# Kernel tuning notes

Measured on AMD Instinct MI355X. Metric: run time of the kernel, lower is better.

## Reference

```python
import jax, jax.numpy as jnp
import numpy as np

G = 8          # n_games
D_IN = 512     # per-game input dim (equal for all games)
H1 = 1024
H2 = 1024
A = 128        # max_actions
B = 8192       # batch rows


def setup_inputs() -> dict:
    key = jax.random.key(0)
    ks = jax.random.split(key, 9)
    state = jax.random.normal(ks[0], (B, D_IN), dtype=jnp.float32)
    idx = jax.random.randint(ks[1], (B,), 0, G, dtype=jnp.int32)
    # per-game input linears: uniform(-1/sqrt(fan_in), 1/sqrt(fan_in))
    lim1 = 1.0 / np.sqrt(D_IN)
    W1 = jax.random.uniform(ks[2], (G, D_IN, H1), minval=-lim1, maxval=lim1, dtype=jnp.float32)
    b1 = jax.random.uniform(ks[3], (G, H1), minval=-lim1, maxval=lim1, dtype=jnp.float32)
    # shared linear
    lim2 = 1.0 / np.sqrt(H1)
    W2 = jax.random.uniform(ks[4], (H1, H2), minval=-lim2, maxval=lim2, dtype=jnp.float32)
    b2 = jax.random.uniform(ks[5], (H2,), minval=-lim2, maxval=lim2, dtype=jnp.float32)
    # per-game output heads: uniform(-0.003, 0.003)
    W3 = jax.random.uniform(ks[6], (G, H2, A), minval=-0.003, maxval=0.003, dtype=jnp.float32)
    b3 = jax.random.uniform(ks[7], (G, A), minval=-0.003, maxval=0.003, dtype=jnp.float32)
    return {"state": state, "idx": idx, "W1": W1, "b1": b1, "W2": W2, "b2": b2, "W3": W3, "b3": b3}


def reference(state, idx, W1, b1, W2, b2, W3, b3):
    # Torch code concatenates per-game groups in sorted-unique-idx order,
    # i.e. a stable permutation of rows by idx; reproduce exactly.
    perm = jnp.argsort(idx, stable=True)          # [B]
    s = state[perm]                               # [B, D_IN]
    g = idx[perm]                                 # [B] game of each permuted row
    # routed first layer: compute all games then gather per-row game
    h1_all = jnp.einsum('bd,gdh->bgh', s, W1) + b1            # [B, G, H1]
    h1 = jax.nn.relu(jnp.take_along_axis(h1_all, g[:, None, None], axis=1)[:, 0, :])  # [B, H1]
    h_f = jax.nn.relu(h1 @ W2 + b2)                            # [B, H2]
    a = jnp.tanh(jnp.einsum('bh,gha->bga', h_f, W3) + b3)      # [B, G, A]
    # NOTE: original gathers heads with the ORIGINAL (unpermuted) idx,
    # even though rows of `a` are in permuted order. Reproduce faithfully.
    out = jnp.take_along_axis(a, idx[:, None, None], axis=1)[:, 0, :]  # [B, A]
    return out
```

## Files before the change

### kernel.cpp

```cpp
#include <hip/hip_runtime.h>
#include <math.h>

#define G_GAMES 8
#define D_IN 512
#define H1 1024
#define H2 1024
#define A_DIM 128
#define B_ROWS 8192

typedef short bf16x8 __attribute__((ext_vector_type(8)));
typedef float f32x4 __attribute__((ext_vector_type(4)));

#define WS_OFF   0u
#define WS_PERM  256u
#define WS_SPERM 33280u
#define WS_W1T   (WS_SPERM + B_ROWS*D_IN*2u)
#define WS_W2T   (WS_W1T + G_GAMES*D_IN*H1*2u)
#define WS_W3T   (WS_W2T + (unsigned)H1*H2*2u)
#define WS_H1    (WS_W3T + G_GAMES*H2*A_DIM*2u)
#define WS_HF    WS_SPERM

__device__ __forceinline__ unsigned short f2bf(float x) {
  union { float f; unsigned int u; } v; v.f = x;
  unsigned int r = v.u + 0x7fffu + ((v.u >> 16) & 1u);
  return (unsigned short)(r >> 16);
}

__device__ __forceinline__ unsigned int cvt_pk_bf16(float lo, float hi) {
  unsigned int r;
  asm("v_cvt_pk_bf16_f32 %0, %1, %2" : "=v"(r) : "v"(lo), "v"(hi));
  return r;
}

__device__ __forceinline__ void async_load16(const void* gptr, void* ldsptr) {
  __builtin_amdgcn_global_load_lds(
      (const __attribute__((address_space(1))) unsigned int*)gptr,
      (__attribute__((address_space(3))) unsigned int*)ldsptr,
      16, 0, 0);
}

__device__ void sort_256(const int* __restrict__ idx, int* __restrict__ perm,
                         int* __restrict__ off) {
  __shared__ int wtot[4][9];
  __shared__ int wbase[4][9];
  __shared__ int offs[9];
  const int t = threadIdx.x, lane = t & 63, wave = t >> 6;
  int my[32];
#pragma unroll
  for (int i = 0; i < 8; ++i) {
    const int4 a = *(const int4*)(idx + t * 32 + i * 4);
    my[i*4+0] = a.x; my[i*4+1] = a.y; my[i*4+2] = a.z; my[i*4+3] = a.w;
  }
  int local[8];
#pragma unroll
  for (int g = 0; g < 8; ++g) {
    int c = 0;
#pragma unroll
    for (int i = 0; i < 32; ++i) c += (my[i] == g) ? 1 : 0;
    local[g] = c;
  }
  int incl[8];
#pragma unroll
  for (int g = 0; g < 8; ++g) {
    int v = local[g];
#pragma unroll
    for (int d = 1; d < 64; d <<= 1) {
      const int n = __shfl_up(v, d);
      if (lane >= d) v += n;
    }
    incl[g] = v;
  }
  if (lane == 63) {
#pragma unroll
    for (int g = 0; g < 8; ++g) wtot[wave][g] = incl[g];
  }
  __syncthreads();
  if (t < 8) {
    int s = 0;
#pragma unroll
    for (int w = 0; w < 4; ++w) { wbase[w][t] = s; s += wtot[w][t]; }
    wtot[0][t] = s;
  }
  __syncthreads();
  if (t == 0) {
    int s = 0;
#pragma unroll
    for (int g = 0; g < 8; ++g) { offs[g] = s; off[g] = s; s += wtot[0][g]; }
    offs[8] = s; off[8] = s;
  }
  __syncthreads();
#pragma unroll
  for (int g = 0; g < 8; ++g) {
    int sg = offs[g] + wbase[wave][g] + (incl[g] - local[g]);
#pragma unroll
    for (int i = 0; i < 32; ++i) {
      const bool m = (my[i] == g);
      if (m) perm[sg] = t * 32 + i;
      sg += m ? 1 : 0;
    }
  }
}

__device__ void trans_tile(const float* __restrict__ in,
                           unsigned short* __restrict__ out,
                           int R, int C, int xt, int yt, int z) {
  in  += (size_t)z * R * C;
  out += (size_t)z * R * C;
  __shared__ unsigned short tl[64][68];
  const int c0 = xt * 64, r0 = yt * 64;
  const int t = threadIdx.x;
#pragma unroll
  for (int pass = 0; pass < 4; ++pass) {
    const int id = pass * 256 + t;
    const int r = id >> 4, f4c = (id & 15) << 2;
    const float4 v = *(const float4*)(in + (size_t)(r0 + r) * C + c0 + f4c);
    uint2 w;
    w.x = cvt_pk_bf16(v.x, v.y);
    w.y = cvt_pk_bf16(v.z, v.w);
    *(uint2*)&tl[r][f4c] = w;
  }
  __syncthreads();
#pragma unroll
  for (int pass = 0; pass < 2; ++pass) {
    const int cc = t >> 2, k0 = ((t & 3) << 3) + (pass << 5);
    unsigned short u[8];
#pragma unroll
    for (int j = 0; j < 8; ++j) u[j] = tl[k0 + j][cc];
    uint4 v;
    v.x = (unsigned)u[0] | ((unsigned)u[1] << 16);
    v.y = (unsigned)u[2] | ((unsigned)u[3] << 16);
    v.z = (unsigned)u[4] | ((unsigned)u[5] << 16);
    v.w = (unsigned)u[6] | ((unsigned)u[7] << 16);
    *(uint4*)(out + (size_t)(c0 + cc) * R + r0 + k0) = v;
  }
}

__global__ __launch_bounds__(256) void k_pre1(const float* __restrict__ W1,
                                              const float* __restrict__ W2,
                                              const float* __restrict__ W3,
                                              const int* __restrict__ idx,
                                              unsigned short* __restrict__ W1T,
                                              unsigned short* __restrict__ W2T,
                                              unsigned short* __restrict__ W3T,
                                              int* __restrict__ perm,
                                              int* __restrict__ off) {
  const int b = blockIdx.x;
  if (b < 1024) {
    const int z = b >> 7, r = b & 127;
    trans_tile(W1, W1T, D_IN, H1, r & 15, r >> 4, z);
  } else if (b < 1280) {
    const int r = b - 1024;
    trans_tile(W2, W2T, H1, H2, r & 15, r >> 4, 0);
  } else if (b < 1536) {
    const int r = (b - 1280) & 31, z = (b - 1280) >> 5;
    trans_tile(W3, W3T, H2, A_DIM, r & 1, r >> 1, z);
  } else {
    sort_256(idx, perm, off);
  }
}

template <int KTOT>
__device__ __forceinline__ void gemm_db_core(const unsigned short* const* aP,
                                             const unsigned short* const* bP,
                                             char* smem, int tid, f32x4 acc[4][4]) {
  const int lane = tid & 63, wave = tid >> 6;
  const int wm = wave & 1, wn = wave >> 1;
  const int sw = lane & 15, quad = lane >> 4;
  const int mA = wm * 64 + sw;
  const int nB = wn * 64 + sw;
  char* A0 = smem;          char* A1 = smem + 16384;
  char* B0 = smem + 32768;  char* B1 = smem + 49152;
  const int NIT = KTOT >> 6;
#pragma unroll
  for (int c = 0; c < 4; ++c) {
    async_load16(aP[c], A0 + (wave * 32 + c * 8) * 128);
    async_load16(bP[c], B0 + (wave * 32 + c * 8) * 128);
  }
#pragma unroll 2
  for (int k = 0; k < NIT; ++k) {
    __syncthreads();
    char* A = (k & 1) ? A1 : A0;
    char* B = (k & 1) ? B1 : B0;
    if (k + 1 < NIT) {
      char* An = (k & 1) ? A0 : A1;
      char* Bn = (k & 1) ? B0 : B1;
      const int koff = (k + 1) << 6;
#pragma unroll
      for (int c = 0; c < 4; ++c) {
        async_load16(aP[c] + koff, An + (wave * 32 + c * 8) * 128);
        async_load16(bP[c] + koff, Bn + (wave * 32 + c * 8) * 128);
      }
    }
#pragma unroll
    for (int ks = 0; ks < 2; ++ks) {
      const int u = ((((ks << 2) + quad) ^ (sw & 7)) << 4);
      bf16x8 aF[4], bF[4];
#pragma unroll
      for (int i = 0; i < 4; ++i) {
        aF[i] = *(const bf16x8*)(A + (mA + i * 16) * 128 + u);
        bF[i] = *(const bf16x8*)(B + (nB + i * 16) * 128 + u);
      }
#pragma unroll
      for (int i = 0; i < 4; ++i)
#pragma unroll
        for (int j = 0; j < 4; ++j)
          acc[i][j] = __builtin_amdgcn_mfma_f32_16x16x32_bf16(aF[i], bF[j], acc[i][j], 0, 0, 0);
    }
  }
}

__device__ __forceinline__ bool seg_map(const int* __restrict__ off, int T,
                                        int& g, int& seg1, int& row0) {
  int base = 0;
  for (int gg = 0; gg < 8; ++gg) {
    const int s = off[gg], e = off[gg + 1];
    const int nt = (e - s + 127) >> 7;
    if (T < base + nt) { g = gg; seg1 = e; row0 = s + (T - base) * 128; return true; }
    base += nt;
  }
  return false;
}

__device__ __forceinline__ bool seg_map32(const int* __restrict__ off, int T,
                                          int& g, int& seg1, int& row0) {
  int base = 0;
  for (int gg = 0; gg < 8; ++gg) {
    const int s = off[gg], e = off[gg + 1];
    const int nt = (e - s + 31) >> 5;
    if (T < base + nt) { g = gg; seg1 = e; row0 = s + (T - base) * 32; return true; }
    base += nt;
  }
  return false;
}

__device__ __forceinline__ void epilogue_bf16(char* smem, const f32x4 acc[4][4],
                                              const float* bj, int tid,
                                              unsigned short* __restrict__ outp,
                                              size_t ldOut, int row0, int col0,
                                              int vrows) {
  const int lane = tid & 63, wave = tid >> 6;
  const int wm = wave & 1, wn = wave >> 1;
  const int sw = lane & 15, quad = lane >> 4;
  __syncthreads();
#pragma unroll
  for (int i = 0; i < 4; ++i)
#pragma unroll
    for (int j = 0; j < 4; ++j)
#pragma unroll
      for (int r = 0; r < 4; ++r) {
        const int row = wm * 64 + i * 16 + quad * 4 + r;
        const int col = wn * 64 + j * 16 + sw;
        const float v = fmaxf(acc[i][j][r] + bj[j], 0.0f);
        *(unsigned short*)(smem + row * 264 + col * 2) = f2bf(v);
      }
  __syncthreads();
#pragma unroll
  for (int q = 0; q < 8; ++q) {
    const int idxq = q * 256 + tid;
    const int row = idxq >> 4, ch = idxq & 15;
    if (row < vrows) {
      const uint2 lo = *(const uint2*)(smem + row * 264 + ch * 16);
      const uint2 hi = *(const uint2*)(smem + row * 264 + ch * 16 + 8);
      uint4 v; v.x = lo.x; v.y = lo.y; v.z = hi.x; v.w = hi.y;
      *(uint4*)((char*)outp + ((size_t)(row0 + row) * ldOut + col0 + ch * 8) * 2) = v;
    }
  }
}

__global__ __launch_bounds__(256, 2) void k_gemm1(const float* __restrict__ state,
                                                  const int* __restrict__ perm,
                                                  const unsigned short* __restrict__ W1T,
                                                  const float* __restrict__ b1,
                                                  const int* __restrict__ off,
                                                  unsigned short* __restrict__ h1out) {
  __shared__ __align__(16) char smem[65536];
  int g, seg1, row0;
  if (!seg_map(off, blockIdx.x, g, seg1, row0)) return;
  const int col0 = blockIdx.y * 128;
  const int tid = threadIdx.x, lane = tid & 63, wave = tid >> 6;
  const int wm = wave & 1, wn = wave >> 1;
  const int sw = lane & 15, quad = lane >> 4;
  const int lc = lane & 7;
  const int gcol = ((lane & 7) ^ (lane >> 3)) << 3;
  const float* aS[4];
  int ldsA[4];
  const unsigned short* bP[4];
#pragma unroll
  for (int c = 0; c < 4; ++c) {
    const int rl = wave * 32 + c * 8 + (lane >> 3);
    int p = row0 + rl;
    if (p > seg1 - 1) p = seg1 - 1;
    aS[c]  = state + (size_t)perm[p] * D_IN + lc * 8;
    ldsA[c] = rl * 128 + ((lc ^ (rl & 7)) << 4);
    bP[c]  = W1T + (size_t)g * H1 * D_IN + (size_t)(col0 + rl) * D_IN + gcol;
  }
  char* A0 = smem;          char* A1 = smem + 16384;
  char* B0 = smem + 32768;  char* B1 = smem + 49152;
  const int mA = wm * 64 + sw, nB = wn * 64 + sw;
  f32x4 acc[4][4] = {};
  {
    float4 t0[4], t1[4];
#pragma unroll
    for (int c = 0; c < 4; ++c) {
      t0[c] = *(const float4*)(aS[c]);
      t1[c] = *(const float4*)(aS[c] + 4);
      async_load16(bP[c], B0 + (wave * 32 + c * 8) * 128);
    }
#pragma unroll
    for (int c = 0; c < 4; ++c) {
      uint4 pk;
      pk.x = cvt_pk_bf16(t0[c].x, t0[c].y);
      pk.y = cvt_pk_bf16(t0[c].z, t0[c].w);
      pk.z = cvt_pk_bf16(t1[c].x, t1[c].y);
      pk.w = cvt_pk_bf16(t1[c].z, t1[c].w);
      *(uint4*)(A0 + ldsA[c]) = pk;
    }
  }
  const int NIT = D_IN >> 6;
#pragma unroll 2
  for (int k = 0; k < NIT; ++k) {
    __syncthreads();
    char* A = (k & 1) ? A1 : A0;
    char* B = (k & 1) ? B1 : B0;
    float4 t0[4], t1[4];
    const bool pf = (k + 1 < NIT);
    if (pf) {
      char* Bn = (k & 1) ? B0 : B1;
      const int koff = (k + 1) << 6;
#pragma unroll
      for (int c = 0; c < 4; ++c) {
        t0[c] = *(const float4*)(aS[c] + koff);
        t1[c] = *(const float4*)(aS[c] + koff + 4);
        async_load16(bP[c] + koff, Bn + (wave * 32 + c * 8) * 128);
      }
    }
#pragma unroll
    for (int ks = 0; ks < 2; ++ks) {
      const int u = ((((ks << 2) + quad) ^ (sw & 7)) << 4);
      bf16x8 aF[4], bF[4];
#pragma unroll
      for (int i = 0; i < 4; ++i) {
        aF[i] = *(const bf16x8*)(A + (mA + i * 16) * 128 + u);
        bF[i] = *(const bf16x8*)(B + (nB + i * 16) * 128 + u);
      }
#pragma unroll
      for (int i = 0; i < 4; ++i)
#pragma unroll
        for (int j = 0; j < 4; ++j)
          acc[i][j] = __builtin_amdgcn_mfma_f32_16x16x32_bf16(aF[i], bF[j], acc[i][j], 0, 0, 0);
    }
    if (pf) {
      char* An = (k & 1) ? A0 : A1;
#pragma unroll
      for (int c = 0; c < 4; ++c) {
        uint4 pk;
        pk.x = cvt_pk_bf16(t0[c].x, t0[c].y);
        pk.y = cvt_pk_bf16(t0[c].z, t0[c].w);
        pk.z = cvt_pk_bf16(t1[c].x, t1[c].y);
        pk.w = cvt_pk_bf16(t1[c].z, t1[c].w);
        *(uint4*)(An + ldsA[c]) = pk;
      }
    }
  }
  const float* bg = b1 + g * H1;
  float bj[4];
#pragma unroll
  for (int j = 0; j < 4; ++j) bj[j] = bg[col0 + wn * 64 + j * 16 + sw];
  const int vrows = min(128, seg1 - row0);
  epilogue_bf16(smem, acc, bj, tid, h1out, H1, row0, col0, vrows);
}

__global__ __launch_bounds__(256) void k_gemm2(const unsigned short* __restrict__ h1in,
                                               const unsigned short* __restrict__ W2T,
                                               const float* __restrict__ b2,
                                               unsigned short* __restrict__ hfout) {
  __shared__ __align__(16) char smem[65536];
  const int row0 = blockIdx.x * 128, col0 = blockIdx.y * 128;
  const int tid = threadIdx.x, lane = tid & 63, wave = tid >> 6;
  const int gcol = ((lane & 7) ^ (lane >> 3)) << 3;
  const unsigned short* aP[4];
  const unsigned short* bP[4];
#pragma unroll
  for (int c = 0; c < 4; ++c) {
    const int rl = wave * 32 + c * 8 + (lane >> 3);
    aP[c] = h1in + (size_t)(row0 + rl) * H1 + gcol;
    bP[c] = W2T + (size_t)(col0 + rl) * H1 + gcol;
  }
  f32x4 acc[4][4] = {};
  gemm_db_core<H1>(aP, bP, smem, tid, acc);
  const int wn = wave >> 1, sw = lane & 15;
  float bj[4];
#pragma unroll
  for (int j = 0; j < 4; ++j) bj[j] = b2[col0 + wn * 64 + j * 16 + sw];
  epilogue_bf16(smem, acc, bj, tid, hfout, H2, row0, col0, 128);
}

__global__ __launch_bounds__(256) void k_gemm3(const unsigned short* __restrict__ hf,
                                               const unsigned short* __restrict__ W3T,
                                               const float* __restrict__ b3,
                                               const int* __restrict__ off,
                                               const int* __restrict__ perm,
                                               float* __restrict__ outp) {
  __shared__ __align__(16) char smem[40960];
  int g, seg1, row0;
  if (!seg_map32(off, blockIdx.x, g, seg1, row0)) return;
  const int tid = threadIdx.x, lane = tid & 63, wave = tid >> 6;
  const int wm = wave & 1, wn = wave >> 1;
  const int sw = lane & 15, quad = lane >> 4;
  const int gcol = ((lane & 7) ^ (lane >> 3)) << 3;
  int q0 = row0 + wave * 8 + (lane >> 3);
  if (q0 > seg1 - 1) q0 = seg1 - 1;
  const unsigned short* aP = hf + (size_t)perm[q0] * H2 + gcol;
  const unsigned short* bP[4];
#pragma unroll
  for (int c = 0; c < 4; ++c) {
    const int rl = wave * 32 + c * 8 + (lane >> 3);
    bP[c] = W3T + (size_t)g * A_DIM * H2 + (size_t)rl * H2 + gcol;
  }
  char* A0 = smem;         char* A1 = smem + 4096;
  char* B0 = smem + 8192;  char* B1 = smem + 24576;
  const int mA = wm * 16 + sw;
  const int nB = wn * 64 + sw;
  f32x4 acc[4] = {};
  async_load16(aP, A0 + (wave * 8) * 128);
#pragma unroll
  for (int c = 0; c < 4; ++c)
    async_load16(bP[c], B0 + (wave * 32 + c * 8) * 128);
#pragma unroll 2
  for (int k = 0; k < (H2 >> 6); ++k) {
    __syncthreads();
    char* A = (k & 1) ? A1 : A0;
    char* B = (k & 1) ? B1 : B0;
    if (k + 1 < (H2 >> 6)) {
      char* An = (k & 1) ? A0 : A1;
      char* Bn = (k & 1) ? B0 : B1;
      const int koff = (k + 1) << 6;
      async_load16(aP + koff, An + (wave * 8) * 128);
#pragma unroll
      for (int c = 0; c < 4; ++c)
        async_load16(bP[c] + koff, Bn + (wave * 32 + c * 8) * 128);
    }
#pragma unroll
    for (int ks = 0; ks < 2; ++ks) {
      const int u = ((((ks << 2) + quad) ^ (sw & 7)) << 4);
      const bf16x8 aF = *(const bf16x8*)(A + mA * 128 + u);
      bf16x8 bF[4];
#pragma unroll
      for (int j = 0; j < 4; ++j)
        bF[j] = *(const bf16x8*)(B + (nB + j * 16) * 128 + u);
#pragma unroll
      for (int j = 0; j < 4; ++j)
        acc[j] = __builtin_amdgcn_mfma_f32_16x16x32_bf16(aF, bF[j], acc[j], 0, 0, 0);
    }
  }
  const float* bg = b3 + g * A_DIM;
  float bj[4];
#pragma unroll
  for (int j = 0; j < 4; ++j) bj[j] = bg[wn * 64 + j * 16 + sw];
  __syncthreads();
#pragma unroll
  for (int j = 0; j < 4; ++j)
#pragma unroll
    for (int r = 0; r < 4; ++r) {
      const int row = wm * 16 + quad * 4 + r;
      const int col = wn * 64 + j * 16 + sw;
      *(float*)(smem + row * 528 + col * 4) = tanhf(acc[j][r] + bj[j]);
    }
  __syncthreads();
#pragma unroll
  for (int qq = 0; qq < 4; ++qq) {
    const int idxq = qq * 256 + tid;
    const int row = idxq >> 5, ch = idxq & 31;
    if (row0 + row < seg1) {
      const uint4 v = *(const uint4*)(smem + row * 528 + ch * 16);
      *(uint4*)((char*)outp + ((size_t)perm[row0 + row] * A_DIM + ch * 4) * 4) = v;
    }
  }
}

extern "C" void kernel_launch(void* const* d_in, const int* in_sizes, int n_in,
                              void* d_out, int out_size, void* d_ws, size_t ws_size,
                              hipStream_t stream) {
  (void)in_sizes; (void)n_in; (void)out_size; (void)ws_size;
  const float* state = (const float*)d_in[0];
  const int*   idx   = (const int*)d_in[1];
  const float* W1    = (const float*)d_in[2];
  const float* b1    = (const float*)d_in[3];
  const float* W2    = (const float*)d_in[4];
  const float* b2    = (const float*)d_in[5];
  const float* W3    = (const float*)d_in[6];
  const float* b3    = (const float*)d_in[7];
  float* outp = (float*)d_out;
  char* ws = (char*)d_ws;
  int* off  = (int*)(ws + WS_OFF);
  int* perm = (int*)(ws + WS_PERM);
  unsigned short* W1T   = (unsigned short*)(ws + WS_W1T);
  unsigned short* W2T   = (unsigned short*)(ws + WS_W2T);
  unsigned short* W3T   = (unsigned short*)(ws + WS_W3T);
  unsigned short* h1    = (unsigned short*)(ws + WS_H1);
  unsigned short* hf    = (unsigned short*)(ws + WS_HF);

  hipLaunchKernelGGL(k_pre1, dim3(1537), dim3(256), 0, stream,
                     W1, W2, W3, idx, W1T, W2T, W3T, perm, off);
  hipLaunchKernelGGL(k_gemm1, dim3(72, 8), dim3(256), 0, stream,
                     state, perm, W1T, b1, off, h1);
  hipLaunchKernelGGL(k_gemm2, dim3(64, 8), dim3(256), 0, stream, h1, W2T, b2, hf);
  hipLaunchKernelGGL(k_gemm3, dim3(264), dim3(256), 0, stream, hf, W3T, b3, off, perm, outp);
}
```

Measured before the change: 163.5 us.

## Switch GEMM1/GEMM2 to single-buffered LDS to fit three blocks per CU

Replaces the double-buffered LDS tiles in the first two GEMM kernels with a single buffer of about 33 KB, so three blocks per CU can be resident instead of two. The launch bounds are raised to match. The aim is to hide global-load latency through more resident waves rather than through software prefetch. In exchange, every K step now waits on a load-then-sync before compute, so load/compute overlap within a block is lost. Register pressure under the three-block launch bound may also limit the gain.

```diff
diff --git a/kernel.cpp b/kernel.cpp
--- a/kernel.cpp
+++ b/kernel.cpp
@@ -160,7 +160,7 @@
 }
 
 template <int KTOT>
-__device__ __forceinline__ void gemm_db_core(const unsigned short* const* aP,
+__device__ __forceinline__ void gemm_sb_core(const unsigned short* const* aP,
                                              const unsigned short* const* bP,
                                              char* smem, int tid, f32x4 acc[4][4]) {
   const int lane = tid & 63, wave = tid >> 6;
@@ -168,29 +168,19 @@
   const int sw = lane & 15, quad = lane >> 4;
   const int mA = wm * 64 + sw;
   const int nB = wn * 64 + sw;
-  char* A0 = smem;          char* A1 = smem + 16384;
-  char* B0 = smem + 32768;  char* B1 = smem + 49152;
+  char* A = smem;
+  char* B = smem + 16384;
   const int NIT = KTOT >> 6;
-#pragma unroll
-  for (int c = 0; c < 4; ++c) {
-    async_load16(aP[c], A0 + (wave * 32 + c * 8) * 128);
-    async_load16(bP[c], B0 + (wave * 32 + c * 8) * 128);
-  }
 #pragma unroll 2
   for (int k = 0; k < NIT; ++k) {
+    if (k) __syncthreads();
+    const int koff = k << 6;
+#pragma unroll
+    for (int c = 0; c < 4; ++c) {
+      async_load16(aP[c] + koff, A + (wave * 32 + c * 8) * 128);
+      async_load16(bP[c] + koff, B + (wave * 32 + c * 8) * 128);
+    }
     __syncthreads();
-    char* A = (k & 1) ? A1 : A0;
-    char* B = (k & 1) ? B1 : B0;
-    if (k + 1 < NIT) {
-      char* An = (k & 1) ? A0 : A1;
-      char* Bn = (k & 1) ? B0 : B1;
-      const int koff = (k + 1) << 6;
-#pragma unroll
-      for (int c = 0; c < 4; ++c) {
-        async_load16(aP[c] + koff, An + (wave * 32 + c * 8) * 128);
-        async_load16(bP[c] + koff, Bn + (wave * 32 + c * 8) * 128);
-      }
-    }
 #pragma unroll
     for (int ks = 0; ks < 2; ++ks) {
       const int u = ((((ks << 2) + quad) ^ (sw & 7)) << 4);
@@ -267,13 +257,13 @@
   }
 }
 
-__global__ __launch_bounds__(256, 2) void k_gemm1(const float* __restrict__ state,
+__global__ __launch_bounds__(256, 3) void k_gemm1(const float* __restrict__ state,
                                                   const int* __restrict__ perm,
                                                   const unsigned short* __restrict__ W1T,
                                                   const float* __restrict__ b1,
                                                   const int* __restrict__ off,
                                                   unsigned short* __restrict__ h1out) {
-  __shared__ __align__(16) char smem[65536];
+  __shared__ __align__(16) char smem[33792];
   int g, seg1, row0;
   if (!seg_map(off, blockIdx.x, g, seg1, row0)) return;
   const int col0 = blockIdx.y * 128;
@@ -294,18 +284,21 @@
     ldsA[c] = rl * 128 + ((lc ^ (rl & 7)) << 4);
     bP[c]  = W1T + (size_t)g * H1 * D_IN + (size_t)(col0 + rl) * D_IN + gcol;
   }
-  char* A0 = smem;          char* A1 = smem + 16384;
-  char* B0 = smem + 32768;  char* B1 = smem + 49152;
+  char* A = smem;
+  char* B = smem + 16384;
   const int mA = wm * 64 + sw, nB = wn * 64 + sw;
   f32x4 acc[4][4] = {};
-  {
-    float4 t0[4], t1[4];
-#pragma unroll
-    for (int c = 0; c < 4; ++c) {
-      t0[c] = *(const float4*)(aS[c]);
-      t1[c] = *(const float4*)(aS[c] + 4);
-      async_load16(bP[c], B0 + (wave * 32 + c * 8) * 128);
-    }
+  const int NIT = D_IN >> 6;
+  float4 t0[4], t1[4];
+#pragma unroll
+  for (int c = 0; c < 4; ++c) {
+    t0[c] = *(const float4*)(aS[c]);
+    t1[c] = *(const float4*)(aS[c] + 4);
+  }
+#pragma unroll 2
+  for (int k = 0; k < NIT; ++k) {
+    if (k) __syncthreads();
+    const int koff = k << 6;
 #pragma unroll
     for (int c = 0; c < 4; ++c) {
       uint4 pk;
@@ -313,25 +306,16 @@
       pk.y = cvt_pk_bf16(t0[c].z, t0[c].w);
       pk.z = cvt_pk_bf16(t1[c].x, t1[c].y);
       pk.w = cvt_pk_bf16(t1[c].z, t1[c].w);
-      *(uint4*)(A0 + ldsA[c]) = pk;
-    }
-  }
-  const int NIT = D_IN >> 6;
-#pragma unroll 2
-  for (int k = 0; k < NIT; ++k) {
+      *(uint4*)(A + ldsA[c]) = pk;
+      async_load16(bP[c] + koff, B + (wave * 32 + c * 8) * 128);
+    }
     __syncthreads();
-    char* A = (k & 1) ? A1 : A0;
-    char* B = (k & 1) ? B1 : B0;
-    float4 t0[4], t1[4];
-    const bool pf = (k + 1 < NIT);
-    if (pf) {
-      char* Bn = (k & 1) ? B0 : B1;
-      const int koff = (k + 1) << 6;
+    if (k + 1 < NIT) {
+      const int koff2 = (k + 1) << 6;
 #pragma unroll
       for (int c = 0; c < 4; ++c) {
-        t0[c] = *(const float4*)(aS[c] + koff);
-        t1[c] = *(const float4*)(aS[c] + koff + 4);
-        async_load16(bP[c] + koff, Bn + (wave * 32 + c * 8) * 128);
+        t0[c] = *(const float4*)(aS[c] + koff2);
+        t1[c] = *(const float4*)(aS[c] + koff2 + 4);
       }
     }
 #pragma unroll
@@ -349,18 +333,6 @@
         for (int j = 0; j < 4; ++j)
           acc[i][j] = __builtin_amdgcn_mfma_f32_16x16x32_bf16(aF[i], bF[j], acc[i][j], 0, 0, 0);
     }
-    if (pf) {
-      char* An = (k & 1) ? A0 : A1;
-#pragma unroll
-      for (int c = 0; c < 4; ++c) {
-        uint4 pk;
-        pk.x = cvt_pk_bf16(t0[c].x, t0[c].y);
-        pk.y = cvt_pk_bf16(t0[c].z, t0[c].w);
-        pk.z = cvt_pk_bf16(t1[c].x, t1[c].y);
-        pk.w = cvt_pk_bf16(t1[c].z, t1[c].w);
-        *(uint4*)(An + ldsA[c]) = pk;
-      }
-    }
   }
   const float* bg = b1 + g * H1;
   float bj[4];
@@ -370,11 +342,11 @@
   epilogue_bf16(smem, acc, bj, tid, h1out, H1, row0, col0, vrows);
 }
 
-__global__ __launch_bounds__(256) void k_gemm2(const unsigned short* __restrict__ h1in,
-                                               const unsigned short* __restrict__ W2T,
-                                               const float* __restrict__ b2,
-                                               unsigned short* __restrict__ hfout) {
-  __shared__ __align__(16) char smem[65536];
+__global__ __launch_bounds__(256, 3) void k_gemm2(const unsigned short* __restrict__ h1in,
+                                                  const unsigned short* __restrict__ W2T,
+                                                  const float* __restrict__ b2,
+                                                  unsigned short* __restrict__ hfout) {
+  __shared__ __align__(16) char smem[33792];
   const int row0 = blockIdx.x * 128, col0 = blockIdx.y * 128;
   const int tid = threadIdx.x, lane = tid & 63, wave = tid >> 6;
   const int gcol = ((lane & 7) ^ (lane >> 3)) << 3;
@@ -387,7 +359,7 @@
     bP[c] = W2T + (size_t)(col0 + rl) * H1 + gcol;
   }
   f32x4 acc[4][4] = {};
-  gemm_db_core<H1>(aP, bP, smem, tid, acc);
+  gemm_sb_core<H1>(aP, bP, smem, tid, acc);
   const int wn = wave >> 1, sw = lane & 15;
   float bj[4];
 #pragma unroll
```

New measurement: 172.1 us. 1.05x slower.
